# Kernel optimization log

Hardware: AMD Instinct MI355X
Metric: run time of the kernel (lower is better)

## Reference

```python
import jax, jax.numpy as jnp
import numpy as np

N_VERTS = 2562


def _uniform(key, shape, bound):
    return jax.random.uniform(key, shape, jnp.float32, -bound, bound)


def vert_align(feat, pos):
    # feat: [B,C,H,W]; pos: [B,N,3], xy in [-1,1] -> bilinear sample -> [B,N,C]
    B, C, H, W = feat.shape
    ft = jnp.transpose(feat, (0, 2, 3, 1))  # [B,H,W,C]
    x = (jnp.clip(pos[..., 0], -1.0, 1.0) + 1.0) * 0.5 * (W - 1)
    y = (jnp.clip(pos[..., 1], -1.0, 1.0) + 1.0) * 0.5 * (H - 1)
    x0 = jnp.floor(x)
    y0 = jnp.floor(y)
    x0i = x0.astype(jnp.int32)
    y0i = y0.astype(jnp.int32)
    x1i = jnp.minimum(x0i + 1, W - 1)
    y1i = jnp.minimum(y0i + 1, H - 1)
    wx = (x - x0)[..., None]
    wy = (y - y0)[..., None]
    b = jnp.arange(B)[:, None]
    f00 = ft[b, y0i, x0i]
    f01 = ft[b, y0i, x1i]
    f10 = ft[b, y1i, x0i]
    f11 = ft[b, y1i, x1i]
    return (f00 * (1 - wx) * (1 - wy) + f01 * wx * (1 - wy)
            + f10 * (1 - wx) * wy + f11 * wx * wy)


def graph_conv(x, adj, w0, w1):
    # relu(x @ w0 + adj @ (x @ w1))
    return jax.nn.relu(x @ w0 + jnp.einsum('bij,bjc->bic', adj, x @ w1))


def setup_inputs() -> dict:
    key = jax.random.key(0)
    ks = jax.random.split(key, 20)
    B, N = 8, N_VERTS
    inp = {
        'conv2_3': jax.random.normal(ks[0], (B, 256, 56, 56), jnp.float32),
        'conv3_4': jax.random.normal(ks[1], (B, 512, 28, 28), jnp.float32),
        'conv4_6': jax.random.normal(ks[2], (B, 1024, 14, 14), jnp.float32),
        'conv5_3': jax.random.normal(ks[3], (B, 2048, 7, 7), jnp.float32),
        # scaled so row sums are O(1), like a normalized dense adjacency
        'vertex_adjacency': jax.random.uniform(ks[4], (B, N, N), jnp.float32) * (2.0 / N),
        'vertex_positions': jax.random.uniform(ks[5], (B, N, 3), jnp.float32) * 2.0 - 1.0,
        'vertex_features': jax.random.normal(ks[6], (B, N, 128), jnp.float32),
    }
    # learned parameters (torch default / GraphConv uniform init)
    inp['w_lin0'] = _uniform(ks[7], (3840, 128), 1.0 / np.sqrt(3840))
    inp['b_lin0'] = _uniform(ks[8], (128,), 1.0 / np.sqrt(3840))
    inp['gc0_w0'] = _uniform(ks[9], (259, 131), 1.0 / np.sqrt(259))
    inp['gc0_w1'] = _uniform(ks[10], (259, 131), 1.0 / np.sqrt(259))
    inp['gc1_w0'] = _uniform(ks[11], (131, 128), 1.0 / np.sqrt(131))
    inp['gc1_w1'] = _uniform(ks[12], (131, 128), 1.0 / np.sqrt(131))
    inp['gc2_w0'] = _uniform(ks[13], (131, 128), 1.0 / np.sqrt(131))
    inp['gc2_w1'] = _uniform(ks[14], (131, 128), 1.0 / np.sqrt(131))
    inp['w_lin1'] = _uniform(ks[15], (128, 3), 1.0 / np.sqrt(128))
    inp['b_lin1'] = _uniform(ks[16], (3,), 1.0 / np.sqrt(128))
    return inp


def reference(conv2_3, conv3_4, conv4_6, conv5_3, vertex_adjacency,
              vertex_positions, vertex_features,
              w_lin0, b_lin0, gc0_w0, gc0_w1, gc1_w0, gc1_w1,
              gc2_w0, gc2_w1, w_lin1, b_lin1):
    verts = jnp.concatenate(
        [vert_align(f, vertex_positions)
         for f in (conv2_3, conv3_4, conv4_6, conv5_3)], axis=2)  # [B,N,3840]
    projected = verts @ w_lin0 + b_lin0                             # [B,N,128]
    vf = jnp.concatenate([vertex_features, vertex_positions, projected], axis=2)  # 259
    h = graph_conv(vf, vertex_adjacency, gc0_w0, gc0_w1)            # [B,N,131]
    h = jnp.concatenate([vertex_positions, h], axis=2)              # 134? no: 3+131=134 -- see note
    h = graph_conv(h[:, :, :131] if h.shape[2] != 131 else h, vertex_adjacency, gc1_w0, gc1_w1)
    h = jnp.concatenate([vertex_positions, h], axis=2)              # 131
    new_features = graph_conv(h, vertex_adjacency, gc2_w0, gc2_w1)  # [B,N,128]
    new_positions = vertex_positions + jnp.tanh(new_features @ w_lin1 + b_lin1)
    return new_positions, new_features
```

## Files before the change

### kernel.cpp

```cpp
#include <hip/hip_runtime.h>
#include <hip/hip_bf16.h>

typedef __attribute__((ext_vector_type(8))) short bf16x8;
typedef __attribute__((ext_vector_type(4))) float f32x4;
typedef __attribute__((ext_vector_type(2))) float f32x2;
typedef long long i64;

static __device__ __forceinline__ float bflo(unsigned v){ return __uint_as_float(v << 16); }
static __device__ __forceinline__ float bfhi(unsigned v){ return __uint_as_float(v & 0xffff0000u); }
static __device__ __forceinline__ unsigned short f2bf(float f){
  unsigned u = __float_as_uint(f);
  u += 0x7FFFu + ((u >> 16) & 1u);
  return (unsigned short)(u >> 16);
}
static __device__ __forceinline__ unsigned f2e4m3(float x){
  unsigned b = __float_as_uint(x);
  unsigned s = (b >> 31) << 7;
  b &= 0x7fffffffu;
  if (b >= 0x43e80000u) return s | 0x7eu;
  if (b < 0x3c800000u)
    return s | (unsigned)rintf(__uint_as_float(b) * 512.f);
  unsigned b2 = b + 0x7ffffu + ((b >> 20) & 1u);
  return s | (((b2 >> 23) - 120u) << 3) | ((b2 >> 20) & 7u);
}
static __device__ __forceinline__ void gload_lds16(const void* g, void* l){
  __builtin_amdgcn_global_load_lds((const __attribute__((address_space(1))) unsigned int*)g,
                                   (__attribute__((address_space(3))) unsigned int*)l, 16, 0, 0);
}

#define MFMA16(acc, a, b) (acc) = __builtin_amdgcn_mfma_f32_16x16x32_bf16((a),(b),(acc),0,0,0)
#define MFMA8(acc, a, b)  (acc) = __builtin_amdgcn_mfma_f32_16x16x32_fp8_fp8((a),(b),(acc),0,0,0)

#define NB    8
#define NVRT  2562
#define MP    2624
#define NRB2  82
#define NRB16 164
#define NKT8  21
#define KOCT  336
#define YO    ((size_t)KOCT*128*8)

#define G_B0 0ul
#define G_B1 3211264ul
#define G_B2 4014080ul
#define G_B3 4214784ul
#define G_TOT 4264960ul

struct PWArgs {
  const float* src[7];
  unsigned short* dst[7];
  int ksrc[7], nsrc[7];
};
__global__ void k_packw_all(PWArgs a)
{
  const int cb[8] = {0,491520,528384,565248,585728,606208,626688,647168};
  int g = blockIdx.x * 256 + threadIdx.x;
#pragma unroll
  for (int s = 0; s < 7; s++){
    if (g >= cb[s] && g < cb[s+1]){
      int li = g - cb[s];
      int k = li >> 7, c = li & 127;
      int ks = a.ksrc[s], ns = a.nsrc[s];
      float v = (k < ks) ? a.src[s][(size_t)k * ns + c] : 0.f;
      a.dst[s][((size_t)(k >> 3) * 128 + c) * 8 + (k & 7)] = f2bf(v);
    }
  }
}

__global__ __launch_bounds__(256) void k_gproj2(
    const float* __restrict__ c0m, const float* __restrict__ c1m,
    const float* __restrict__ c2m, const float* __restrict__ c3m,
    const unsigned short* __restrict__ wp,
    unsigned short* __restrict__ G)
{
  __shared__ f32x4 red[3][1024];
  int bx = blockIdx.x;
  int m, b, tile;
  if (bx < 784)      { m = 0; b = bx / 98;  tile = bx - b*98; }
  else if (bx < 984) { int l = bx-784;  m = 1; b = l / 25; tile = l - b*25; }
  else if (bx < 1040){ int l = bx-984;  m = 2; b = l / 7;  tile = l - b*7; }
  else               { int l = bx-1040; m = 3; b = l >> 1; tile = l & 1; }
  int C  = 256 << m;
  int HW = (m==0)?3136:(m==1)?784:(m==2)?196:49;
  const float* src = ((m==0)?c0m:(m==1)?c1m:(m==2)?c2m:c3m) + (size_t)b * C * HW;
  size_t gb = ((m==0)?G_B0:(m==1)?G_B1:(m==2)?G_B2:G_B3) + (size_t)b * HW * 128;
  int ko8 = (m==0)?0:(m==1)?32:(m==2)?96:224;

  int t = threadIdx.x, w = t >> 6, lane = t & 63;
  int l15 = lane & 15, l4 = lane >> 4;
  int hw0 = tile * 32;
  int ar0 = min(hw0 + l15, HW - 1);
  int ar1 = min(hw0 + 16 + l15, HW - 1);

  f32x4 acc[2][8];
#pragma unroll
  for (int i = 0; i < 2; i++)
#pragma unroll
    for (int j = 0; j < 8; j++) acc[i][j] = (f32x4){0,0,0,0};

  int kq = C >> 2;
  int kbeg = w * kq, klim = kbeg + kq;
  for (int kb = kbeg; kb < klim; kb += 32){
    bf16x8 a0, a1;
#pragma unroll
    for (int j = 0; j < 8; j++){
      int cc = kb + l4*8 + j;
      a0[j] = (short)f2bf(src[(size_t)cc * HW + ar0]);
      a1[j] = (short)f2bf(src[(size_t)cc * HW + ar1]);
    }
    size_t bo = ((size_t)(ko8 + (kb>>3) + l4) * 128 + l15) * 8;
#pragma unroll
    for (int cf = 0; cf < 8; cf++){
      bf16x8 bb = *(const bf16x8*)(wp + bo + cf*128);
      MFMA16(acc[0][cf], a0, bb);
      MFMA16(acc[1][cf], a1, bb);
    }
  }

  if (w){
#pragma unroll
    for (int rf = 0; rf < 2; rf++)
#pragma unroll
      for (int cf = 0; cf < 8; cf++)
        red[w-1][(rf*8+cf)*64 + lane] = acc[rf][cf];
  }
  __syncthreads();
  if (!w){
#pragma unroll
    for (int rf = 0; rf < 2; rf++)
#pragma unroll
      for (int cf = 0; cf < 8; cf++){
        int i = (rf*8+cf)*64 + lane;
        f32x4 s = acc[rf][cf] + red[0][i] + red[1][i] + red[2][i];
        int col = cf*16 + l15;
#pragma unroll
        for (int r = 0; r < 4; r++){
          int hw = hw0 + rf*16 + l4*4 + r;
          if (hw < HW) G[gb + (size_t)hw*128 + col] = f2bf(s[r]);
        }
      }
  }
}

__global__ void k_prep2(const float* __restrict__ vfeat, const float* __restrict__ pos,
                        const unsigned short* __restrict__ G,
                        const float* __restrict__ bias,
                        unsigned short* __restrict__ vf,
                        unsigned short* __restrict__ x1,
                        unsigned short* __restrict__ x2,
                        unsigned char* __restrict__ y1p8)
{
  int b = blockIdx.y;
  if (blockIdx.x == 0){
    unsigned long long* z = (unsigned long long*)(y1p8 + (size_t)b*YO + (size_t)328*128*8);
    int i = threadIdx.x;
    z[i*4+0] = 0; z[i*4+1] = 0; z[i*4+2] = 0; z[i*4+3] = 0;
  }
  int row = blockIdx.x * 4 + (threadIdx.x >> 6);
  int lane = threadIdx.x & 63;
  size_t vfo = ((size_t)b * MP + row) * 288;
  size_t xo  = ((size_t)b * MP + row) * 160;
  if (row < NVRT){
    size_t src = (size_t)b * NVRT + row;
    float px = fminf(fmaxf(pos[src*3 + 0], -1.f), 1.f);
    float py = fminf(fmaxf(pos[src*3 + 1], -1.f), 1.f);
    int c0 = lane * 2;
    float s0 = bias[c0], s1 = bias[c0 + 1];
#pragma unroll
    for (int m = 0; m < 4; m++){
      int W = 56 >> m;
      int HW = W * W;
      size_t gb = (m==0)?G_B0:(m==1)?G_B1:(m==2)?G_B2:G_B3;
      float gx = (px + 1.f) * 0.5f * (float)(W - 1);
      float gy = (py + 1.f) * 0.5f * (float)(W - 1);
      int x0 = (int)floorf(gx), y0 = (int)floorf(gy);
      float wx = gx - (float)x0, wy = gy - (float)y0;
      int x1i = min(x0 + 1, W - 1), y1i = min(y0 + 1, W - 1);
      const unsigned short* g = G + gb + (size_t)b * HW * 128;
      unsigned v00 = *(const unsigned*)(g + ((size_t)(y0 *W + x0 ))*128 + c0);
      unsigned v01 = *(const unsigned*)(g + ((size_t)(y0 *W + x1i))*128 + c0);
      unsigned v10 = *(const unsigned*)(g + ((size_t)(y1i*W + x0 ))*128 + c0);
      unsigned v11 = *(const unsigned*)(g + ((size_t)(y1i*W + x1i))*128 + c0);
      float w00 = (1.f-wx)*(1.f-wy), w01 = wx*(1.f-wy);
      float w10 = (1.f-wx)*wy,       w11 = wx*wy;
      s0 += w00*bflo(v00) + w01*bflo(v01) + w10*bflo(v10) + w11*bflo(v11);
      s1 += w00*bfhi(v00) + w01*bfhi(v01) + w10*bfhi(v10) + w11*bfhi(v11);
    }
    vf[vfo + 131 + c0]     = f2bf(s0);
    vf[vfo + 131 + c0 + 1] = f2bf(s1);
    float2 fv = *(const float2*)(vfeat + src*128 + c0);
    vf[vfo + c0]     = f2bf(fv.x);
    vf[vfo + c0 + 1] = f2bf(fv.y);
    if (lane < 3){
      unsigned short v = f2bf(pos[src*3 + lane]);
      vf[vfo + 128 + lane] = v;
      x1[xo + lane] = v;
      x2[xo + lane] = v;
    }
    if (lane >= 32 && lane < 61) vf[vfo + 259 + (lane - 32)] = 0;
    if (lane < 29){ x1[xo + 131 + lane] = 0; x2[xo + 131 + lane] = 0; }
  } else {
    for (int c = lane; c < 288; c += 64) vf[vfo + c] = 0;
    for (int c = lane; c < 160; c += 64){ x1[xo + c] = 0; x2[xo + c] = 0; }
  }
}

__global__ void k_adjpack8(const float* __restrict__ adj, unsigned char* __restrict__ adjP)
{
  int kt = blockIdx.x, rb = blockIdx.y, b = blockIdx.z;
  int t = threadIdx.x;
  int r = t >> 4, kseg = t & 15;
  int grow = rb*16 + r, gk = kt*128 + kseg*8;
  float v[8];
  if (grow < NVRT && gk + 8 <= NVRT){
    const float4* p = (const float4*)(adj + ((size_t)b*NVRT + grow)*NVRT + gk);
    float4 f0 = p[0], f1 = p[1];
    v[0]=f0.x; v[1]=f0.y; v[2]=f0.z; v[3]=f0.w;
    v[4]=f1.x; v[5]=f1.y; v[6]=f1.z; v[7]=f1.w;
  } else if (grow < NVRT){
    const float* ap = adj + ((size_t)b*NVRT + grow)*NVRT;
#pragma unroll
    for (int e = 0; e < 8; e++){ int k = gk + e; v[e] = (k < NVRT) ? ap[k] : 0.f; }
  } else {
#pragma unroll
    for (int e = 0; e < 8; e++) v[e] = 0.f;
  }
  unsigned long long q = 0;
#pragma unroll
  for (int e = 0; e < 8; e++)
    q |= (unsigned long long)f2e4m3(v[e] * 1024.f) << (8*e);
  unsigned char* tb = adjP + (((size_t)b*NRB16 + rb)*NKT8 + kt) * 2048;
  *(unsigned long long*)(tb + 128*r + 8*(kseg ^ r)) = q;
}

template<int KX>
__global__ __launch_bounds__(256) void k_y1(
    const unsigned short* __restrict__ x,
    const unsigned short* __restrict__ wp1,
    unsigned char* __restrict__ y1p8)
{
  int b = blockIdx.y, rb = blockIdx.x * 32;
  int t = threadIdx.x, wave = t >> 6, lane = t & 63;
  int rf = wave & 1, ch = wave >> 1;
  int l15 = lane & 15, l4 = lane >> 4;
  f32x4 a1[4];
#pragma unroll
  for (int c = 0; c < 4; c++) a1[c] = (f32x4){0,0,0,0};
  int row = rb + rf*16 + l15;
  const unsigned short* xp = x + ((size_t)b * MP + row) * KX + l4 * 8;
#pragma unroll
  for (int kb = 0; kb < KX; kb += 32){
    bf16x8 a = *(const bf16x8*)(xp + kb);
    size_t bo = ((size_t)((kb>>3) + l4) * 128 + ch*64 + l15) * 8;
#pragma unroll
    for (int c = 0; c < 4; c++){
      bf16x8 b1 = *(const bf16x8*)(wp1 + bo + c*128);
      MFMA16(a1[c], a, b1);
    }
  }
  unsigned char* yb = y1p8 + (size_t)b * YO;
#pragma unroll
  for (int c = 0; c < 4; c++){
    int col = ch*64 + c*16 + l15;
    int orow0 = rb + rf*16 + l4*4;
    unsigned q = f2e4m3(a1[c][0]) | (f2e4m3(a1[c][1]) << 8)
               | (f2e4m3(a1[c][2]) << 16) | (f2e4m3(a1[c][3]) << 24);
    *(unsigned*)(yb + ((size_t)(orow0 >> 3) * 128 + col) * 8 + (orow0 & 7)) = q;
  }
}

template<int EPI, int KX>
__global__ __launch_bounds__(256) void k_adj8(
    const unsigned char* __restrict__ adjP,
    const unsigned char* __restrict__ y1p8,
    const unsigned short* __restrict__ x,
    const unsigned short* __restrict__ wp0,
    unsigned short* __restrict__ xnext,
    float* __restrict__ outf,
    const float* __restrict__ pos,
    const float* __restrict__ wl1, const float* __restrict__ bl1,
    float* __restrict__ opos)
{
  __shared__ __align__(16) unsigned char abuf[2][2048];
  __shared__ float hbuf[16][128];
  int rb = blockIdx.x, b = blockIdx.y;
  int t = threadIdx.x, w = t >> 6, lane = t & 63;
  int l15 = lane & 15, l4 = lane >> 4;
  const unsigned char* tb = adjP + (((size_t)b*NRB16 + rb)*NKT8) * 2048;
  const unsigned char* yb = y1p8 + (size_t)b * YO;

  f32x4 acc[2], accW[2];
  acc[0] = (f32x4){0,0,0,0};  acc[1] = (f32x4){0,0,0,0};
  accW[0] = (f32x4){0,0,0,0}; accW[1] = (f32x4){0,0,0,0};

  auto stage = [&](int kt, int bufi){
    if (w < 2)
      gload_lds16(tb + (size_t)kt*2048 + w*1024 + lane*16, &abuf[bufi][w*1024]);
  };

  stage(0, 0);

  const unsigned short* xr = x + ((size_t)b*MP + rb*16 + l15)*KX + l4*8;
#pragma unroll
  for (int kb = 0; kb < KX; kb += 32){
    bf16x8 ax = *(const bf16x8*)(xr + kb);
    size_t bo = ((size_t)((kb>>3) + l4)*128 + w*32 + l15)*8;
    MFMA16(accW[0], ax, *(const bf16x8*)(wp0 + bo));
    MFMA16(accW[1], ax, *(const bf16x8*)(wp0 + bo + 128));
  }

  __syncthreads();

  for (int kt = 0; kt < NKT8; ++kt){
    int cur = kt & 1;
    if (kt < NKT8-1) stage(kt+1, cur ^ 1);
    const unsigned char* ab = &abuf[cur][0];
#pragma unroll
    for (int sel = 0; sel < 2; sel++){
#pragma unroll
      for (int ks = 0; ks < 2; ks++){
        int koct = sel*8 + ks*4 + l4;
        i64 a = *(const i64*)(ab + 128*l15 + 8*(koct ^ l15));
        const unsigned char* bp = yb + ((size_t)(kt*16 + koct)*128 + w*32 + l15)*8;
        i64 b0 = *(const i64*)(bp);
        i64 b1 = *(const i64*)(bp + 128);
        MFMA8(acc[0], a, b0);
        MFMA8(acc[1], a, b1);
      }
    }
    __syncthreads();
  }

#pragma unroll
  for (int cf = 0; cf < 2; cf++){
    int col = w*32 + cf*16 + l15;
#pragma unroll
    for (int r = 0; r < 4; r++){
      int row16 = l4*4 + r;
      int row = rb*16 + row16;
      float v = fmaxf(accW[cf][r] + acc[cf][r] * 0.0009765625f, 0.f);
      if (EPI == 0){
        if (row < NVRT) xnext[((size_t)b*MP + row)*160 + 3 + col] = f2bf(v);
      } else {
        if (row < NVRT) outf[((size_t)b*NVRT + row)*128 + col] = v;
        hbuf[row16][col] = v;
      }
    }
  }

  if (EPI == 1){
    __syncthreads();
#pragma unroll
    for (int rr = 0; rr < 4; rr++){
      int row16 = w*4 + rr;
      int grow = rb*16 + row16;
      if (grow < NVRT){
        int c0 = lane * 2;
        float v0 = hbuf[row16][c0], v1 = hbuf[row16][c0+1];
        float p[3];
#pragma unroll
        for (int j = 0; j < 3; j++){
          p[j] = v0 * wl1[c0*3 + j] + v1 * wl1[c0*3 + 3 + j];
#pragma unroll
          for (int off = 1; off < 64; off <<= 1)
            p[j] += __shfl_xor(p[j], off);
        }
        if (lane == 0){
          size_t po = ((size_t)b * NVRT + grow) * 3;
#pragma unroll
          for (int j = 0; j < 3; j++)
            opos[po + j] = pos[po + j] + tanhf(p[j] + bl1[j]);
        }
      }
    }
  }
}

extern "C" void kernel_launch(void* const* d_in, const int* in_sizes, int n_in,
                              void* d_out, int out_size, void* d_ws, size_t ws_size,
                              hipStream_t stream)
{
  const float* conv[4] = {(const float*)d_in[0], (const float*)d_in[1],
                          (const float*)d_in[2], (const float*)d_in[3]};
  const float* adj   = (const float*)d_in[4];
  const float* pos   = (const float*)d_in[5];
  const float* vfeat = (const float*)d_in[6];
  const float* wlin0 = (const float*)d_in[7];
  const float* blin0 = (const float*)d_in[8];
  const float* gw[6] = {(const float*)d_in[9],  (const float*)d_in[10],
                        (const float*)d_in[11], (const float*)d_in[12],
                        (const float*)d_in[13], (const float*)d_in[14]};
  const float* wlin1 = (const float*)d_in[15];
  const float* blin1 = (const float*)d_in[16];

  char* ws = (char*)d_ws;
  size_t off = 0;
  auto take = [&](size_t bytes)->char* {
    char* p = ws + off;
    off += (bytes + 255) & ~(size_t)255;
    return p;
  };
  unsigned short* G    = (unsigned short*)take(G_TOT * 2);
  unsigned char*  adjP = (unsigned char*)take((size_t)NB*NRB16*NKT8*2048);
  unsigned short* wl0p = (unsigned short*)take((size_t)3840*128*2);
  unsigned short* w0p0 = (unsigned short*)take((size_t)288*128*2);
  unsigned short* w1p0 = (unsigned short*)take((size_t)288*128*2);
  unsigned short* w0p1 = (unsigned short*)take((size_t)160*128*2);
  unsigned short* w1p1 = (unsigned short*)take((size_t)160*128*2);
  unsigned short* w0p2 = (unsigned short*)take((size_t)160*128*2);
  unsigned short* w1p2 = (unsigned short*)take((size_t)160*128*2);
  unsigned short* vf   = (unsigned short*)take((size_t)NB*MP*288*2);
  unsigned short* x1   = (unsigned short*)take((size_t)NB*MP*160*2);
  unsigned short* x2   = (unsigned short*)take((size_t)NB*MP*160*2);
  unsigned char*  y1p8 = (unsigned char*)take((size_t)NB*YO);

  float* out_pos  = (float*)d_out;
  float* out_feat = out_pos + (size_t)NB*NVRT*3;

  PWArgs pw;
  pw.src[0]=wlin0; pw.dst[0]=wl0p; pw.ksrc[0]=3840; pw.nsrc[0]=128;
  pw.src[1]=gw[0]; pw.dst[1]=w0p0; pw.ksrc[1]=259;  pw.nsrc[1]=131;
  pw.src[2]=gw[1]; pw.dst[2]=w1p0; pw.ksrc[2]=259;  pw.nsrc[2]=131;
  pw.src[3]=gw[2]; pw.dst[3]=w0p1; pw.ksrc[3]=131;  pw.nsrc[3]=128;
  pw.src[4]=gw[3]; pw.dst[4]=w1p1; pw.ksrc[4]=131;  pw.nsrc[4]=128;
  pw.src[5]=gw[4]; pw.dst[5]=w0p2; pw.ksrc[5]=131;  pw.nsrc[5]=128;
  pw.src[6]=gw[5]; pw.dst[6]=w1p2; pw.ksrc[6]=131;  pw.nsrc[6]=128;
  k_packw_all<<<2528, 256, 0, stream>>>(pw);
  k_gproj2<<<1056, 256, 0, stream>>>(conv[0], conv[1], conv[2], conv[3], wl0p, G);
  k_prep2<<<dim3(MP/4, NB), 256, 0, stream>>>(vfeat, pos, G, blin0, vf, x1, x2, y1p8);
  k_adjpack8<<<dim3(NKT8, NRB16, NB), 256, 0, stream>>>(adj, adjP);
  k_y1<288><<<dim3(NRB2, NB), 256, 0, stream>>>(vf, w1p0, y1p8);
  k_adj8<0,288><<<dim3(NRB16, NB), 256, 0, stream>>>(adjP, y1p8, vf, w0p0, x1, nullptr, nullptr, nullptr, nullptr, nullptr);
  k_y1<160><<<dim3(NRB2, NB), 256, 0, stream>>>(x1, w1p1, y1p8);
  k_adj8<0,160><<<dim3(NRB16, NB), 256, 0, stream>>>(adjP, y1p8, x1, w0p1, x2, nullptr, nullptr, nullptr, nullptr, nullptr);
  k_y1<160><<<dim3(NRB2, NB), 256, 0, stream>>>(x2, w1p2, y1p8);
  k_adj8<1,160><<<dim3(NRB16, NB), 256, 0, stream>>>(adjP, y1p8, x2, w0p2, nullptr, out_feat, pos, wlin1, blin1, out_pos);
  (void)in_sizes; (void)n_in; (void)out_size; (void)ws_size;
}
```

Baseline: 270.6 us.

## Fuse next-layer Y1 projection into adjacency kernel epilogue with ping-pong buffers

Each non-final adjacency GEMM kernel now builds the next layer's input row tile (positions plus relu output, padded) in shared memory. It multiplies that tile by the next layer's W1 and writes the fp8 Y1 buffer directly, which removes two separate k_y1 launches and their re-read of x. Y1 buffers alternate between two workspace allocations so a kernel never overwrites the buffer it is reading. This adds epilogue MFMA work and extra shared memory per block in the adjacency kernels.

```diff
diff --git a/kernel.cpp b/kernel.cpp
--- a/kernel.cpp
+++ b/kernel.cpp
@@ -148,13 +148,16 @@
                         unsigned short* __restrict__ vf,
                         unsigned short* __restrict__ x1,
                         unsigned short* __restrict__ x2,
-                        unsigned char* __restrict__ y1p8)
+                        unsigned char* __restrict__ y1A,
+                        unsigned char* __restrict__ y1B)
 {
   int b = blockIdx.y;
   if (blockIdx.x == 0){
-    unsigned long long* z = (unsigned long long*)(y1p8 + (size_t)b*YO + (size_t)328*128*8);
+    unsigned long long* za = (unsigned long long*)(y1A + (size_t)b*YO + (size_t)328*128*8);
+    unsigned long long* zb = (unsigned long long*)(y1B + (size_t)b*YO + (size_t)328*128*8);
     int i = threadIdx.x;
-    z[i*4+0] = 0; z[i*4+1] = 0; z[i*4+2] = 0; z[i*4+3] = 0;
+#pragma unroll
+    for (int j = 0; j < 4; j++){ za[i*4+j] = 0; zb[i*4+j] = 0; }
   }
   int row = blockIdx.x * 4 + (threadIdx.x >> 6);
   int lane = threadIdx.x & 63;
@@ -272,22 +275,25 @@
 template<int EPI, int KX>
 __global__ __launch_bounds__(256) void k_adj8(
     const unsigned char* __restrict__ adjP,
-    const unsigned char* __restrict__ y1p8,
+    const unsigned char* __restrict__ y1in,
     const unsigned short* __restrict__ x,
     const unsigned short* __restrict__ wp0,
+    const unsigned short* __restrict__ wp1n,
+    unsigned char* __restrict__ y1out,
+    const float* __restrict__ posg,
     unsigned short* __restrict__ xnext,
     float* __restrict__ outf,
-    const float* __restrict__ pos,
     const float* __restrict__ wl1, const float* __restrict__ bl1,
     float* __restrict__ opos)
 {
   __shared__ __align__(16) unsigned char abuf[2][2048];
-  __shared__ float hbuf[16][128];
+  __shared__ unsigned short xbuf[EPI == 0 ? 16 : 1][168];
+  __shared__ float hbuf[EPI == 1 ? 16 : 1][128];
   int rb = blockIdx.x, b = blockIdx.y;
   int t = threadIdx.x, w = t >> 6, lane = t & 63;
   int l15 = lane & 15, l4 = lane >> 4;
   const unsigned char* tb = adjP + (((size_t)b*NRB16 + rb)*NKT8) * 2048;
-  const unsigned char* yb = y1p8 + (size_t)b * YO;
+  const unsigned char* yb = y1in + (size_t)b * YO;
 
   f32x4 acc[2], accW[2];
   acc[0] = (f32x4){0,0,0,0};  acc[1] = (f32x4){0,0,0,0};
@@ -299,6 +305,20 @@
   };
 
   stage(0, 0);
+
+  if (EPI == 0){
+    if (t < 48){
+      int r16 = t / 3, c = t - r16*3;
+      int grow = rb*16 + r16;
+      xbuf[r16][c] = (grow < NVRT) ? f2bf(posg[((size_t)b*NVRT + grow)*3 + c]) : 0;
+    }
+    {
+      int r16 = t >> 4, c0 = 131 + (t & 15);
+      xbuf[r16][c0] = 0;
+      if (c0 + 16 < 168) xbuf[r16][c0 + 16] = 0;
+      if (c0 + 32 < 168) xbuf[r16][c0 + 32] = 0;
+    }
+  }
 
   const unsigned short* xr = x + ((size_t)b*MP + rb*16 + l15)*KX + l4*8;
 #pragma unroll
@@ -340,16 +360,37 @@
       int row = rb*16 + row16;
       float v = fmaxf(accW[cf][r] + acc[cf][r] * 0.0009765625f, 0.f);
       if (EPI == 0){
-        if (row < NVRT) xnext[((size_t)b*MP + row)*160 + 3 + col] = f2bf(v);
+        unsigned short hb = f2bf(v);
+        if (row < NVRT) xnext[((size_t)b*MP + row)*160 + 3 + col] = hb;
+        xbuf[row16][3 + col] = hb;
       } else {
         if (row < NVRT) outf[((size_t)b*NVRT + row)*128 + col] = v;
         hbuf[row16][col] = v;
       }
     }
   }
-
-  if (EPI == 1){
-    __syncthreads();
+  __syncthreads();
+
+  if (EPI == 0){
+    f32x4 accY[2];
+    accY[0] = (f32x4){0,0,0,0}; accY[1] = (f32x4){0,0,0,0};
+#pragma unroll
+    for (int ks = 0; ks < 5; ks++){
+      bf16x8 a = *(const bf16x8*)(&xbuf[l15][ks*32 + l4*8]);
+      size_t bo = ((size_t)(ks*4 + l4)*128 + w*32 + l15)*8;
+      MFMA16(accY[0], a, *(const bf16x8*)(wp1n + bo));
+      MFMA16(accY[1], a, *(const bf16x8*)(wp1n + bo + 128));
+    }
+    unsigned char* yo = y1out + (size_t)b * YO;
+#pragma unroll
+    for (int cf = 0; cf < 2; cf++){
+      int col = w*32 + cf*16 + l15;
+      int orow0 = rb*16 + l4*4;
+      unsigned q = f2e4m3(accY[cf][0]) | (f2e4m3(accY[cf][1]) << 8)
+                 | (f2e4m3(accY[cf][2]) << 16) | (f2e4m3(accY[cf][3]) << 24);
+      *(unsigned*)(yo + ((size_t)(orow0 >> 3) * 128 + col) * 8 + (orow0 & 7)) = q;
+    }
+  } else {
 #pragma unroll
     for (int rr = 0; rr < 4; rr++){
       int row16 = w*4 + rr;
@@ -369,7 +410,7 @@
           size_t po = ((size_t)b * NVRT + grow) * 3;
 #pragma unroll
           for (int j = 0; j < 3; j++)
-            opos[po + j] = pos[po + j] + tanhf(p[j] + bl1[j]);
+            opos[po + j] = posg[po + j] + tanhf(p[j] + bl1[j]);
         }
       }
     }
@@ -412,7 +453,8 @@
   unsigned short* vf   = (unsigned short*)take((size_t)NB*MP*288*2);
   unsigned short* x1   = (unsigned short*)take((size_t)NB*MP*160*2);
   unsigned short* x2   = (unsigned short*)take((size_t)NB*MP*160*2);
-  unsigned char*  y1p8 = (unsigned char*)take((size_t)NB*YO);
+  unsigned char*  y1A  = (unsigned char*)take((size_t)NB*YO);
+  unsigned char*  y1B  = (unsigned char*)take((size_t)NB*YO);
 
   float* out_pos  = (float*)d_out;
   float* out_feat = out_pos + (size_t)NB*NVRT*3;
@@ -427,13 +469,14 @@
   pw.src[6]=gw[5]; pw.dst[6]=w1p2; pw.ksrc[6]=131;  pw.nsrc[6]=128;
   k_packw_all<<<2528, 256, 0, stream>>>(pw);
   k_gproj2<<<1056, 256, 0, stream>>>(conv[0], conv[1], conv[2], conv[3], wl0p, G);
-  k_prep2<<<dim3(MP/4, NB), 256, 0, stream>>>(vfeat, pos, G, blin0, vf, x1, x2, y1p8);
+  k_prep2<<<dim3(MP/4, NB), 256, 0, stream>>>(vfeat, pos, G, blin0, vf, x1, x2, y1A, y1B);
   k_adjpack8<<<dim3(NKT8, NRB16, NB), 256, 0, stream>>>(adj, adjP);
-  k_y1<288><<<dim3(NRB2, NB), 256, 0, stream>>>(vf, w1p0, y1p8);
-  k_adj8<0,288><<<dim3(NRB16, NB), 256, 0, stream>>>(adjP, y1p8, vf, w0p0, x1, nullptr, nullptr, nullptr, nullptr, nullptr);
-  k_y1<160><<<dim3(NRB2, NB), 256, 0, stream>>>(x1, w1p1, y1p8);
-  k_adj8<0,160><<<dim3(NRB16, NB), 256, 0, stream>>>(adjP, y1p8, x1, w0p1, x2, nullptr, nullptr, nullptr, nullptr, nullptr);
-  k_y1<160><<<dim3(NRB2, NB), 256, 0, stream>>>(x2, w1p2, y1p8);
-  k_adj8<1,160><<<dim3(NRB16, NB), 256, 0, stream>>>(adjP, y1p8, x2, w0p2, nullptr, out_feat, pos, wlin1, blin1, out_pos);
+  k_y1<288><<<dim3(NRB2, NB), 256, 0, stream>>>(vf, w1p0, y1A);
+  k_adj8<0,288><<<dim3(NRB16, NB), 256, 0, stream>>>(adjP, y1A, vf, w0p0, w1p1, y1B, pos,
+                                                     x1, nullptr, nullptr, nullptr, nullptr);
+  k_adj8<0,160><<<dim3(NRB16, NB), 256, 0, stream>>>(adjP, y1B, x1, w0p1, w1p2, y1A, pos,
+                                                     x2, nullptr, nullptr, nullptr, nullptr);
+  k_adj8<1,160><<<dim3(NRB16, NB), 256, 0, stream>>>(adjP, y1A, x2, w0p2, nullptr, nullptr, pos,
+                                                     nullptr, out_feat, wlin1, blin1, out_pos);
   (void)in_sizes; (void)n_in; (void)out_size; (void)ws_size;
 }
```

Result: faster. 262.2 us (-3.1%).
